# Performance work log

Measured on AMD Instinct MI355X. Metric: run time of the kernel, lower is better.

The kernel has to match this reference:

```python
import jax, jax.numpy as jnp
from jax import lax
import numpy as np

VOCAB, EMBED, HID = 128, 256, 1024
BATCH, SEQ = 64, 1024


def setup_inputs() -> dict:
    key = jax.random.key(0)
    ks = jax.random.split(key, 8)
    s = 0.05  # small init scale so tanh/sigmoid gates are not saturated
    return {
        "ids": jax.random.randint(ks[0], (BATCH, SEQ), 0, VOCAB, dtype=jnp.int32),
        "emb": jax.random.normal(ks[1], (VOCAB, EMBED), jnp.float32) * s,
        "w_in": jax.random.normal(ks[2], (EMBED, 3 * HID), jnp.float32) * s,
        "b_in": jnp.zeros((3 * HID,), jnp.float32),
        "w_rec": jax.random.normal(ks[3], (HID, 3 * HID), jnp.float32) * s,
        "b_rec": jnp.zeros((3 * HID,), jnp.float32),
        "w_out": jax.random.normal(ks[4], (HID, VOCAB), jnp.float32) * s,
        "b_out": jnp.zeros((VOCAB,), jnp.float32),
    }


def reference(ids, emb, w_in, b_in, w_rec, b_rec, w_out, b_out):
    # Embedding lookup: [B,T,E]
    x = emb[ids]
    # Input-side gate pre-activations computed for all timesteps at once: [B,T,3H]
    xg = x @ w_in + b_in
    B = x.shape[0]
    H = w_rec.shape[0]
    h0 = jnp.zeros((B, H), x.dtype)  # gru.get_initial_state -> zeros

    def step(h, xg_t):
        # Keras GRU, reset_after=True: recurrent bias added BEFORE reset-gate product
        rg = h @ w_rec + b_rec                      # [B,3H]
        xz, xr, xh = jnp.split(xg_t, 3, axis=-1)
        rz, rr, rh = jnp.split(rg, 3, axis=-1)
        z = jax.nn.sigmoid(xz + rz)                 # update gate
        r = jax.nn.sigmoid(xr + rr)                 # reset gate
        hh = jnp.tanh(xh + r * rh)                  # candidate
        h_new = z * h + (1.0 - z) * hh
        return h_new, h_new

    _, hs = lax.scan(step, h0, jnp.swapaxes(xg, 0, 1))  # hs: [T,B,H]
    hs = jnp.swapaxes(hs, 0, 1)                          # [B,T,H]
    logits = hs @ w_out + b_out                          # [B,T,V]
    return logits
```

## Files before the change

### kernel.cpp

```cpp
#include <hip/hip_runtime.h>
#include <hip/hip_bf16.h>
#include <hip/hip_fp16.h>
#include <cstddef>


#define VOCABN 128
#define HIDN   1024
#define BN     64
#define TN     1024
#define C3N    3072
#define NREP   2

typedef _Float16 half8 __attribute__((ext_vector_type(8)));
typedef float    f32x4 __attribute__((ext_vector_type(4)));
typedef unsigned int u32x4 __attribute__((ext_vector_type(4)));
typedef unsigned int u32x2 __attribute__((ext_vector_type(2)));

__global__ __launch_bounds__(256, 1) void emb_gemm(
    const float* __restrict__ emb, const float* __restrict__ w_in,
    const float* __restrict__ b_in, _Float16* __restrict__ Mtab)
{
    __shared__ float se[16][256];
    const int tid = threadIdx.x;
    const int c   = blockIdx.x * 256 + tid;
    const int v0  = blockIdx.y * 16;
#pragma unroll
    for (int i = 0; i < 16; ++i) {
        int flat = i * 256 + tid;
        int r = flat >> 8, e = flat & 255;
        se[r][e] = emb[(v0 + r) * 256 + e];
    }
    __syncthreads();
    float acc[16];
#pragma unroll
    for (int r = 0; r < 16; ++r) acc[r] = 0.f;
    for (int e = 0; e < 256; ++e) {
        float w = w_in[(size_t)e * C3N + c];
#pragma unroll
        for (int r = 0; r < 16; ++r) acc[r] = fmaf(se[r][e], w, acc[r]);
    }
    float bc = b_in[c];
#pragma unroll
    for (int r = 0; r < 16; ++r)
        Mtab[(size_t)(v0 + r) * C3N + c] = (_Float16)(acc[r] + bc);
}

__global__ __launch_bounds__(64, 1) void gru_persist(
    const int* __restrict__ ids, const _Float16* __restrict__ Mtab_g,
    const float* __restrict__ w_rec, const float* __restrict__ b_rec,
    _Float16* __restrict__ comm,
    unsigned int* __restrict__ flags,
    _Float16* __restrict__ hs)
{
    __shared__ _Float16 wh[32 * 64 * 8];
    __shared__ _Float16 mtab[VOCABN * 48];
    __shared__ __align__(16) _Float16 sht[256];
    const half8* whp = (const half8*)wh;

    const int l  = threadIdx.x;
    const int w  = blockIdx.x & 63;
    const int mt = blockIdx.x >> 6;
    const int jj = l & 15;
    const int lh = l >> 4;

    for (int i = 0; i < 256; ++i) {
        int flat = i * 64 + l;
        int e  = flat & 7;
        int ll = (flat >> 3) & 63;
        int kt = flat >> 9;
        int k   = kt * 32 + (ll >> 4) * 8 + e;
        int col = 2048 + w * 16 + (ll & 15);
        wh[(kt * 64 + ll) * 8 + e] = (_Float16)w_rec[(size_t)k * C3N + col];
    }
    for (int i = 0; i < 96; ++i) {
        int flat = i * 64 + l;
        int v = flat / 48, c = flat % 48;
        int col = (c >> 4) * 1024 + w * 16 + (c & 15);
        mtab[v * 48 + c] = Mtab_g[(size_t)v * C3N + col];
    }
    half8 wz[32], wr[32];
#pragma unroll
    for (int kt = 0; kt < 32; ++kt) {
#pragma unroll
        for (int e = 0; e < 8; ++e) {
            int k = kt * 32 + lh * 8 + e;
            wz[kt][e] = (_Float16)w_rec[(size_t)k * C3N + w * 16 + jj];
            wr[kt][e] = (_Float16)w_rec[(size_t)k * C3N + 1024 + w * 16 + jj];
        }
    }
    const float bz = b_rec[w * 16 + jj];
    const float br = b_rec[1024 + w * 16 + jj];
    const float bh = b_rec[2048 + w * 16 + jj];
    __syncthreads();

    const int bbase = mt * 16 + lh * 4;
    float hprev[4] = {0.f, 0.f, 0.f, 0.f};

    const int ktp = w >> 1;
    _Float16* cw_base = comm + (size_t)mt * 16384 + ktp * 512
                      + (w & 1) * 256 + l * 4;
    const _Float16* cr_base = comm + (size_t)(w & 1) * 131072
                            + (size_t)mt * 16384 + (size_t)l * 8;
    unsigned int* myflag = flags + (w * 4 + mt) * 16;
    const unsigned int* pollp = flags + (w & 1) * 4096 + (l * 4 + mt) * 16;

    int idsv[4];
#pragma unroll
    for (int q = 0; q < 4; ++q) idsv[q] = ids[(size_t)(bbase + q) * TN];

#define ISSUE(BUF, G) do { _Pragma("unroll")                                  \
    for (int i_ = 0; i_ < 8; ++i_)                                            \
        asm volatile("global_load_dwordx4 %0, %1, off sc0 sc1"                \
            : "=v"(BUF[i_]) : "v"(crd + (8*(G)+i_) * 512) : "memory");        \
    } while (0)

#define WAITN(N) do {                                                         \
    asm volatile("s_waitcnt vmcnt(" #N ")" ::: "memory");                     \
    __builtin_amdgcn_sched_barrier(0); } while (0)

#define PROCG(BUF, G) do { _Pragma("unroll")                                  \
    for (int i_ = 0; i_ < 8; ++i_) {                                          \
        half8 a_ = __builtin_bit_cast(half8, BUF[i_]);                        \
        int kt_ = 8*(G) + i_;                                                 \
        acc0 = __builtin_amdgcn_mfma_f32_16x16x32_f16(a_, wz[kt_], acc0, 0, 0, 0); \
        acc1 = __builtin_amdgcn_mfma_f32_16x16x32_f16(a_, wr[kt_], acc1, 0, 0, 0); \
        acc2 = __builtin_amdgcn_mfma_f32_16x16x32_f16(a_, whp[kt_ * 64 + l], acc2, 0, 0, 0); \
    } } while (0)

    for (int t = 0; t < TN; ++t) {
        {
            const unsigned int tv = (unsigned int)t;
            while (true) {
                unsigned int f;
                asm volatile("global_load_dword %0, %1, off sc0 sc1\n\t"
                             "s_waitcnt vmcnt(0)"
                             : "=v"(f) : "v"(pollp) : "memory");
                if (__all(f >= tv)) break;
                __builtin_amdgcn_s_sleep(1);
            }
        }
        __builtin_amdgcn_sched_barrier(0);

        const _Float16* crd = cr_base + (size_t)(t & 1) * 65536;
        u32x4 bA[8], bB[8], bC[8];
        f32x4 acc0 = {0.f, 0.f, 0.f, 0.f};
        f32x4 acc1 = {0.f, 0.f, 0.f, 0.f};
        f32x4 acc2 = {0.f, 0.f, 0.f, 0.f};

        ISSUE(bA, 0); ISSUE(bB, 1); ISSUE(bC, 2);
        WAITN(16); PROCG(bA, 0); ISSUE(bA, 3);
        WAITN(16); PROCG(bB, 1);
        WAITN(8);  PROCG(bC, 2);
        WAITN(0);  PROCG(bA, 3);

        float hnv[4];
#pragma unroll
        for (int q = 0; q < 4; ++q) {
            float az = acc0[q], ar = acc1[q], ah = acc2[q];
            int id = idsv[q];
            float xz = (float)mtab[id * 48 + jj];
            float xr = (float)mtab[id * 48 + 16 + jj];
            float xh = (float)mtab[id * 48 + 32 + jj];
            float z  = 1.f / (1.f + __expf(-(xz + az + bz)));
            float r  = 1.f / (1.f + __expf(-(xr + ar + br)));
            float hh = tanhf(xh + r * (ah + bh));
            float hn = z * hprev[q] + (1.f - z) * hh;
            hprev[q] = hn;
            hnv[q] = hn;
        }
#pragma unroll
        for (int q = 0; q < 4; ++q)
            sht[(lh * 4 + q) * 16 + jj] = (_Float16)hnv[q];
        asm volatile("s_waitcnt lgkmcnt(0)" ::: "memory");
        __builtin_amdgcn_sched_barrier(0);
        {
            const int B   = (l >> 1) & 15;
            const int jj0 = 8 * (l >> 5) + (l & 1) * 4;
            u32x2 pk = *(const u32x2*)&sht[B * 16 + jj0];
            _Float16* cwp = cw_base + (size_t)((t + 1) & 1) * 65536;
#pragma unroll
            for (int rr = 0; rr < NREP; ++rr)
                asm volatile("global_store_dwordx2 %0, %1, off sc0 sc1"
                             :: "v"(cwp + rr * 131072), "v"(pk) : "memory");
        }
#pragma unroll
        for (int q = 0; q < 4; ++q)
            hs[((size_t)t * BN + (bbase + q)) * HIDN + w * 16 + jj] = (_Float16)hnv[q];
        if (t + 1 < TN) {
#pragma unroll
            for (int q = 0; q < 4; ++q)
                idsv[q] = ids[(size_t)(bbase + q) * TN + t + 1];
        }
        WAITN(8);
        if (l == 0) {
            unsigned int fv = (unsigned int)(t + 1);
#pragma unroll
            for (int rr = 0; rr < NREP; ++rr)
                asm volatile("global_store_dword %0, %1, off sc0 sc1"
                             :: "v"(myflag + rr * 4096), "v"(fv) : "memory");
        }
    }
#undef ISSUE
#undef WAITN
#undef PROCG
}

__global__ __launch_bounds__(256, 2) void out_gemm(
    const _Float16* __restrict__ hs, const float* __restrict__ w_out,
    const float* __restrict__ b_out, float* __restrict__ out)
{
    __shared__ float sa[16][1024];
    const int tid = threadIdx.x;
    const int m0  = blockIdx.x * 16;
#pragma unroll
    for (int i = 0; i < 8; ++i) {
        int flat = i * 256 + tid;
        int r = flat >> 7, kc = flat & 127;
        half8 hv = *(const half8*)(hs + (size_t)(m0 + r) * 1024 + kc * 8);
#pragma unroll
        for (int e = 0; e < 8; ++e) sa[r][kc * 8 + e] = (float)hv[e];
    }
    __syncthreads();
    const int v = tid & 127, g = tid >> 7;
    float acc[8];
#pragma unroll
    for (int r = 0; r < 8; ++r) acc[r] = 0.f;
    for (int k = 0; k < 1024; ++k) {
        float wv = w_out[(size_t)k * VOCABN + v];
#pragma unroll
        for (int r = 0; r < 8; ++r) acc[r] = fmaf(sa[g * 8 + r][k], wv, acc[r]);
    }
    float bo = b_out[v];
#pragma unroll
    for (int r = 0; r < 8; ++r) {
        int m = m0 + g * 8 + r;
        out[((size_t)(m & 63) * TN + (m >> 6)) * VOCABN + v] = acc[r] + bo;
    }
}

extern "C" void kernel_launch(void* const* d_in, const int* in_sizes, int n_in,
                              void* d_out, int out_size, void* d_ws, size_t ws_size,
                              hipStream_t stream) {
    const int*   ids   = (const int*)d_in[0];
    const float* emb   = (const float*)d_in[1];
    const float* w_in  = (const float*)d_in[2];
    const float* b_in  = (const float*)d_in[3];
    const float* w_rec = (const float*)d_in[4];
    const float* b_rec = (const float*)d_in[5];
    const float* w_out = (const float*)d_in[6];
    const float* b_out = (const float*)d_in[7];
    float* out = (float*)d_out;

    char* ws = (char*)d_ws;
    _Float16* Mtab = (_Float16*)ws;
    size_t off = (size_t)VOCABN * C3N * 2;
    _Float16* comm = (_Float16*)(ws + off); off += (size_t)NREP * 131072 * 2;
    unsigned int* flags = (unsigned int*)(ws + off); off += NREP * 4096 * 4;
    _Float16* hs = (_Float16*)(ws + off);

    emb_gemm<<<dim3(12, 8), 256, 0, stream>>>(emb, w_in, b_in, Mtab);
    hipMemsetAsync(comm, 0, (size_t)NREP * 131072 * 2, stream);
    hipMemsetAsync(flags, 0, NREP * 4096 * 4, stream);

    gru_persist<<<256, 64, 0, stream>>>(ids, Mtab, w_rec, b_rec,
                                        comm, flags, hs);
    out_gemm<<<(BN * TN) / 16, 256, 0, stream>>>(hs, w_out, b_out, out);
}
```

Baseline: 4.611 ms.

## Fuse output projection into persistent GRU kernel, overlapping it via flag polling

Merges the output GEMM into the persistent GRU launch as extra blocks that poll a third replica of per-timestep flags and compute logits for timestep t once every GRU block has published h_t. The hidden-state store becomes a system-coherent write issued before the flag update, so the waiting blocks can read it. The aim is to hide the separate out_gemm pass behind the latency-bound recurrence. The cost is that GRU blocks now launch with 256 threads, 192 of which exit immediately, plus extra flag stores per step. GEMM blocks spinning and competing for CUs could also slow the recurrence or affect whether all blocks stay co-resident.

```diff
diff --git a/kernel.cpp b/kernel.cpp
--- a/kernel.cpp
+++ b/kernel.cpp
@@ -10,6 +10,8 @@
 #define TN     1024
 #define C3N    3072
 #define NREP   2
+#define FREP   3
+#define NGRU   256
 
 typedef _Float16 half8 __attribute__((ext_vector_type(8)));
 typedef float    f32x4 __attribute__((ext_vector_type(4)));
@@ -45,19 +47,75 @@
         Mtab[(size_t)(v0 + r) * C3N + c] = (_Float16)(acc[r] + bc);
 }
 
-__global__ __launch_bounds__(64, 1) void gru_persist(
+__global__ __launch_bounds__(256, 1) void fused_persist(
     const int* __restrict__ ids, const _Float16* __restrict__ Mtab_g,
     const float* __restrict__ w_rec, const float* __restrict__ b_rec,
     _Float16* __restrict__ comm,
     unsigned int* __restrict__ flags,
-    _Float16* __restrict__ hs)
+    _Float16* __restrict__ hs,
+    const float* __restrict__ w_out, const float* __restrict__ b_out,
+    float* __restrict__ out)
 {
-    __shared__ _Float16 wh[32 * 64 * 8];
-    __shared__ _Float16 mtab[VOCABN * 48];
-    __shared__ __align__(16) _Float16 sht[256];
+    __shared__ __align__(16) char smem[46080];
+    _Float16* wh   = (_Float16*)smem;
+    _Float16* mtab = (_Float16*)(smem + 32768);
+    _Float16* sht  = (_Float16*)(smem + 45056);
     const half8* whp = (const half8*)wh;
 
-    const int l  = threadIdx.x;
+    const int tid = threadIdx.x;
+
+    if (blockIdx.x >= NGRU) {
+        _Float16* sa = (_Float16*)smem;
+        const int bid = blockIdx.x - NGRU;
+        const int m0  = bid * 16;
+        const int tn  = m0 >> 6;
+        const int pl  = (m0 >> 4) & 3;
+        if (tid < 64) {
+            const unsigned int* pollp = flags + 2 * 4096 + (tid * 4 + pl) * 16;
+            const unsigned int tv = (unsigned int)(tn + 1);
+            while (true) {
+                unsigned int f;
+                asm volatile("global_load_dword %0, %1, off sc0 sc1\n\t"
+                             "s_waitcnt vmcnt(0)"
+                             : "=v"(f) : "v"(pollp) : "memory");
+                if (__all(f >= tv)) break;
+                __builtin_amdgcn_s_sleep(32);
+            }
+        }
+        __syncthreads();
+#pragma unroll
+        for (int i = 0; i < 8; ++i) {
+            int flat = i * 256 + tid;
+            int r = flat >> 7, kc = flat & 127;
+            const _Float16* p = hs + (size_t)(m0 + r) * HIDN + kc * 8;
+            u32x4 hv;
+            asm volatile("global_load_dword" "x4 %0, %1, off sc0 sc1\n\t"
+                         "s_waitcnt vmcnt(0)"
+                         : "=v"(hv) : "v"(p) : "memory");
+            *(u32x4*)(sa + (size_t)r * HIDN + kc * 8) = hv;
+        }
+        __syncthreads();
+        const int v = tid & 127, g = tid >> 7;
+        float acc[8];
+#pragma unroll
+        for (int r = 0; r < 8; ++r) acc[r] = 0.f;
+        for (int k = 0; k < 1024; ++k) {
+            float wv = w_out[(size_t)k * VOCABN + v];
+#pragma unroll
+            for (int r = 0; r < 8; ++r)
+                acc[r] = fmaf((float)sa[(size_t)(g * 8 + r) * HIDN + k], wv, acc[r]);
+        }
+        float bo = b_out[v];
+#pragma unroll
+        for (int r = 0; r < 8; ++r) {
+            int m = m0 + g * 8 + r;
+            out[((size_t)(m & 63) * TN + (m >> 6)) * VOCABN + v] = acc[r] + bo;
+        }
+        return;
+    }
+
+    if (tid >= 64) return;
+    const int l  = tid;
     const int w  = blockIdx.x & 63;
     const int mt = blockIdx.x >> 6;
     const int jj = l & 15;
@@ -91,7 +149,8 @@
     const float bz = b_rec[w * 16 + jj];
     const float br = b_rec[1024 + w * 16 + jj];
     const float bh = b_rec[2048 + w * 16 + jj];
-    __syncthreads();
+    asm volatile("s_waitcnt lgkmcnt(0)" ::: "memory");
+    __builtin_amdgcn_sched_barrier(0);
 
     const int bbase = mt * 16 + lh * 4;
     float hprev[4] = {0.f, 0.f, 0.f, 0.f};
@@ -169,6 +228,14 @@
             hnv[q] = hn;
         }
 #pragma unroll
+        for (int q = 0; q < 4; ++q) {
+            unsigned int hv16 = (unsigned int)__builtin_bit_cast(
+                unsigned short, (_Float16)hnv[q]);
+            _Float16* hp = hs + ((size_t)t * BN + (bbase + q)) * HIDN + w * 16 + jj;
+            asm volatile("global_store_short %0, %1, off sc0 sc1"
+                         :: "v"(hp), "v"(hv16) : "memory");
+        }
+#pragma unroll
         for (int q = 0; q < 4; ++q)
             sht[(lh * 4 + q) * 16 + jj] = (_Float16)hnv[q];
         asm volatile("s_waitcnt lgkmcnt(0)" ::: "memory");
@@ -183,19 +250,18 @@
                 asm volatile("global_store_dwordx2 %0, %1, off sc0 sc1"
                              :: "v"(cwp + rr * 131072), "v"(pk) : "memory");
         }
-#pragma unroll
-        for (int q = 0; q < 4; ++q)
-            hs[((size_t)t * BN + (bbase + q)) * HIDN + w * 16 + jj] = (_Float16)hnv[q];
         if (t + 1 < TN) {
 #pragma unroll
             for (int q = 0; q < 4; ++q)
                 idsv[q] = ids[(size_t)(bbase + q) * TN + t + 1];
-        }
-        WAITN(8);
+            WAITN(4);
+        } else {
+            WAITN(0);
+        }
         if (l == 0) {
             unsigned int fv = (unsigned int)(t + 1);
 #pragma unroll
-            for (int rr = 0; rr < NREP; ++rr)
+            for (int rr = 0; rr < FREP; ++rr)
                 asm volatile("global_store_dword %0, %1, off sc0 sc1"
                              :: "v"(myflag + rr * 4096), "v"(fv) : "memory");
         }
@@ -203,39 +269,6 @@
 #undef ISSUE
 #undef WAITN
 #undef PROCG
-}
-
-__global__ __launch_bounds__(256, 2) void out_gemm(
-    const _Float16* __restrict__ hs, const float* __restrict__ w_out,
-    const float* __restrict__ b_out, float* __restrict__ out)
-{
-    __shared__ float sa[16][1024];
-    const int tid = threadIdx.x;
-    const int m0  = blockIdx.x * 16;
-#pragma unroll
-    for (int i = 0; i < 8; ++i) {
-        int flat = i * 256 + tid;
-        int r = flat >> 7, kc = flat & 127;
-        half8 hv = *(const half8*)(hs + (size_t)(m0 + r) * 1024 + kc * 8);
-#pragma unroll
-        for (int e = 0; e < 8; ++e) sa[r][kc * 8 + e] = (float)hv[e];
-    }
-    __syncthreads();
-    const int v = tid & 127, g = tid >> 7;
-    float acc[8];
-#pragma unroll
-    for (int r = 0; r < 8; ++r) acc[r] = 0.f;
-    for (int k = 0; k < 1024; ++k) {
-        float wv = w_out[(size_t)k * VOCABN + v];
-#pragma unroll
-        for (int r = 0; r < 8; ++r) acc[r] = fmaf(sa[g * 8 + r][k], wv, acc[r]);
-    }
-    float bo = b_out[v];
-#pragma unroll
-    for (int r = 0; r < 8; ++r) {
-        int m = m0 + g * 8 + r;
-        out[((size_t)(m & 63) * TN + (m >> 6)) * VOCABN + v] = acc[r] + bo;
-    }
 }
 
 extern "C" void kernel_launch(void* const* d_in, const int* in_sizes, int n_in,
@@ -255,14 +288,13 @@
     _Float16* Mtab = (_Float16*)ws;
     size_t off = (size_t)VOCABN * C3N * 2;
     _Float16* comm = (_Float16*)(ws + off); off += (size_t)NREP * 131072 * 2;
-    unsigned int* flags = (unsigned int*)(ws + off); off += NREP * 4096 * 4;
+    unsigned int* flags = (unsigned int*)(ws + off); off += FREP * 4096 * 4;
     _Float16* hs = (_Float16*)(ws + off);
 
     emb_gemm<<<dim3(12, 8), 256, 0, stream>>>(emb, w_in, b_in, Mtab);
     hipMemsetAsync(comm, 0, (size_t)NREP * 131072 * 2, stream);
-    hipMemsetAsync(flags, 0, NREP * 4096 * 4, stream);
-
-    gru_persist<<<256, 64, 0, stream>>>(ids, Mtab, w_rec, b_rec,
-                                        comm, flags, hs);
-    out_gemm<<<(BN * TN) / 16, 256, 0, stream>>>(hs, w_out, b_out, out);
+    hipMemsetAsync(flags, 0, FREP * 4096 * 4, stream);
+
+    fused_persist<<<NGRU + (BN * TN) / 16, 256, 0, stream>>>(
+        ids, Mtab, w_rec, b_rec, comm, flags, hs, w_out, b_out, out);
 }
```

Result: no change. 4.684 ms (+1.6%).
